# Kernel tuning notes

Measured on AMD Instinct MI355X. Metric: run time of the kernel, lower is better.

Reference implementation:

```python
import jax, jax.numpy as jnp
import numpy as np

N, M, D = 20000, 16000, 128

def setup_inputs() -> dict:
    key = jax.random.key(0)
    ks = jax.random.split(key, 4)
    return {
        "clear_feature": jax.random.normal(ks[0], (N, D), dtype=jnp.float32),
        "rain_feature": jax.random.normal(ks[1], (M, D), dtype=jnp.float32),
        # torch nn.Linear weight layout: (out_features, in_features)
        "W1": jax.random.normal(ks[2], (D, 2 * D), dtype=jnp.float32) * 0.05,
        "b1": jnp.zeros((D,), dtype=jnp.float32),
        "W2": jax.random.normal(ks[3], (1, D), dtype=jnp.float32) * 0.05,
        "b2": jnp.zeros((1,), dtype=jnp.float32),
    }

def reference(clear_feature, rain_feature, W1, b1, W2, b2):
    # --- KNN alignment (k=1): argmin of squared Euclidean distance == cdist+topk(smallest) ---
    x2 = jnp.sum(clear_feature * clear_feature, axis=-1, keepdims=True)   # [N,1]
    y2 = jnp.sum(rain_feature * rain_feature, axis=-1)                    # [M]
    d2 = x2 + y2 - 2.0 * (clear_feature @ rain_feature.T)                 # [N,M]
    idx = jnp.argmin(d2, axis=-1)                                         # [N]
    aligned = rain_feature[idx]                                           # [N,D] gather
    # --- attention MLP: Linear(2D->D) + ReLU + Linear(D->1) + Sigmoid ---
    comb = jnp.concatenate([clear_feature, aligned], axis=-1)             # [N,2D]
    h = jax.nn.relu(comb @ W1.T + b1)                                     # [N,D]
    w = jax.nn.sigmoid(h @ W2.T + b2)                                     # [N,1]
    # --- gated fusion ---
    return w * clear_feature + (1.0 - w) * aligned
```

## Files before the change

### kernel.cpp

```cpp
#include <hip/hip_runtime.h>
#include <stdint.h>

#define NN 20000
#define MM 16000
#define DD 128
#define CT 500
#define SPLITS 32
#define RBG 157

typedef unsigned long long u64;
typedef _Float16 f16x8 __attribute__((ext_vector_type(8)));
typedef float f32x16 __attribute__((ext_vector_type(16)));

__global__ void k_y2(const float* __restrict__ rain, float* __restrict__ y2) {
    int row = blockIdx.x * 4 + (threadIdx.x >> 6);
    int lane = threadIdx.x & 63;
    if (row >= MM) return;
    float2 v = ((const float2*)(rain + (size_t)row * DD))[lane];
    float s = v.x * v.x + v.y * v.y;
    #pragma unroll
    for (int off = 32; off > 0; off >>= 1) s += __shfl_down(s, off);
    if (lane == 0) y2[row] = s;
}

__global__ void k_split_B(const float* __restrict__ rain, _Float16* __restrict__ Bimg) {
    int id = blockIdx.x * 256 + threadIdx.x;
    if (id >= CT * 512) return;
    int cl = id & 31;
    int kh = (id >> 5) & 1;
    int ks = (id >> 6) & 7;
    int tc = id >> 9;
    int m = tc * 32 + cl;
    const float4* src = (const float4*)(rain + (size_t)m * DD + ks * 16 + kh * 8);
    float4 v0 = src[0], v1 = src[1];
    float x[8] = {v0.x, v0.y, v0.z, v0.w, v1.x, v1.y, v1.z, v1.w};
    _Float16 hi[8], lo[8];
    #pragma unroll
    for (int j = 0; j < 8; ++j) {
        _Float16 h = (_Float16)x[j];
        hi[j] = h;
        lo[j] = (_Float16)(x[j] - (float)h);
    }
    int chunk = (ks * 2 + kh) * 32 + cl;
    size_t base = (size_t)tc * 8192;
    *(f16x8*)(Bimg + base + (size_t)chunk * 8) = *(f16x8*)hi;
    *(f16x8*)(Bimg + base + 4096 + (size_t)chunk * 8) = *(f16x8*)lo;
}

__global__ void k_w1img(const float* __restrict__ W1, _Float16* __restrict__ W1img) {
    int id = blockIdx.x * 256 + threadIdx.x;
    if (id >= 4096) return;
    int cl = id & 31;
    int kh = (id >> 5) & 1;
    int cg = (id >> 6) & 3;
    int ks = id >> 8;
    int d = cg * 32 + cl;
    int k = ks * 16 + kh * 8;
    const float4* src = (const float4*)(W1 + (size_t)d * 256 + k);
    float4 v0 = src[0], v1 = src[1];
    float x[8] = {v0.x, v0.y, v0.z, v0.w, v1.x, v1.y, v1.z, v1.w};
    _Float16 h[8];
    #pragma unroll
    for (int j = 0; j < 8; ++j) h[j] = (_Float16)x[j];
    *(f16x8*)(W1img + (size_t)id * 8) = *(f16x8*)h;
}

__global__ __launch_bounds__(256, 3) void k_dist(
        const float* __restrict__ clear_f,
        const _Float16* __restrict__ Bimg, const float* __restrict__ y2,
        u64* __restrict__ keys2) {
    __shared__ _Float16 lds[2][8192];
    __shared__ float y2s[512];

    const int tid = threadIdx.x;
    const int w = tid >> 6, lane = tid & 63;
    const int l5 = lane >> 5, l31 = lane & 31;
    const int b = blockIdx.x;
    const int split = b & 31;
    const int n0 = (b >> 5) * 128;
    const int nt = (CT - split + SPLITS - 1) / SPLITS;

    #define STAGE(T, BUF) do {                                                 \
        const _Float16* gsrc_ = Bimg + (size_t)(T) * 8192;                     \
        _Float16* dst_ = &lds[BUF][0];                                         \
        _Pragma("unroll")                                                      \
        for (int n_ = 0; n_ < 4; ++n_) {                                       \
            int seg_ = w * 4 + n_;                                             \
            __builtin_amdgcn_global_load_lds(                                  \
                (const __attribute__((address_space(1))) unsigned int*)        \
                    (gsrc_ + (size_t)seg_ * 512 + (size_t)lane * 8),           \
                (__attribute__((address_space(3))) unsigned int*)              \
                    (dst_ + (size_t)seg_ * 512),                               \
                16, 0, 0);                                                     \
        }                                                                      \
    } while (0)

    STAGE(split, 0);

    for (int j = tid; j < nt * 32; j += 256) {
        int tt = j >> 5;
        int cc = j & 31;
        y2s[j] = y2[(split + tt * SPLITS) * 32 + cc];
    }

    f16x8 afh[8], afl[8];
    {
        int r = n0 + w * 32 + l31;
        if (r >= NN) r = NN - 1;
        const float* ap = clear_f + (size_t)r * DD + l5 * 8;
        #pragma unroll
        for (int ks = 0; ks < 8; ++ks) {
            float4 v0 = *(const float4*)(ap + ks * 16);
            float4 v1 = *(const float4*)(ap + ks * 16 + 4);
            float x[8] = {v0.x, v0.y, v0.z, v0.w, v1.x, v1.y, v1.z, v1.w};
            _Float16 hi[8], lo[8];
            #pragma unroll
            for (int j = 0; j < 8; ++j) {
                float s = -2.f * x[j];
                _Float16 h = (_Float16)s;
                hi[j] = h;
                lo[j] = (_Float16)(s - (float)h);
            }
            afh[ks] = *(f16x8*)hi;
            afl[ks] = *(f16x8*)lo;
        }
    }

    __syncthreads();

    float bestd[16];
    unsigned bits[2] = {0u, 0u};
    #pragma unroll
    for (int s = 0; s < 16; ++s) bestd[s] = 1e30f;

    int p = 0;
    for (int i = 0; i < nt; ++i) {
        if (i + 1 < nt) STAGE(split + (i + 1) * SPLITS, 1 - p);

        float y2v = y2s[i * 32 + l31];

        f32x16 accA, accB;
        #pragma unroll
        for (int e = 0; e < 16; ++e) { accA[e] = y2v; accB[e] = 0.f; }

        const _Float16* lbuf = &lds[p][0];
        #pragma unroll
        for (int ks = 0; ks < 8; ++ks) {
            f16x8 bh = *(const f16x8*)(lbuf + (size_t)ks * 512 + (size_t)lane * 8);
            f16x8 bl = *(const f16x8*)(lbuf + 4096 + (size_t)ks * 512 + (size_t)lane * 8);
            __builtin_amdgcn_s_setprio(1);
            accA = __builtin_amdgcn_mfma_f32_32x32x16_f16(afh[ks], bh, accA, 0, 0, 0);
            accB = __builtin_amdgcn_mfma_f32_32x32x16_f16(afl[ks], bh, accB, 0, 0, 0);
            accA = __builtin_amdgcn_mfma_f32_32x32x16_f16(afh[ks], bl, accA, 0, 0, 0);
            __builtin_amdgcn_s_setprio(0);
        }

        const unsigned nib = (unsigned)i;
        #pragma unroll
        for (int e = 0; e < 16; ++e) {
            float d = accA[e] + accB[e];
            int sh = 4 * (e & 7);
            bool up = d < bestd[e];
            bestd[e] = up ? d : bestd[e];
            bits[e >> 3] = up ? ((bits[e >> 3] & ~(15u << sh)) | (nib << sh))
                              : bits[e >> 3];
        }

        __syncthreads();
        p ^= 1;
    }
    #undef STAGE

    #pragma unroll
    for (int s = 0; s < 16; ++s) {
        unsigned nib = (bits[s >> 3] >> (4 * (s & 7))) & 15u;
        int col = (split + (int)nib * SPLITS) * 32 + l31;
        unsigned u = __float_as_uint(bestd[s]);
        u = (u & 0x80000000u) ? ~u : (u | 0x80000000u);
        u64 key = ((u64)u << 32) | (unsigned)col;
        #pragma unroll
        for (int off = 1; off < 32; off <<= 1) {
            u64 o = __shfl_xor(key, off);
            if (o < key) key = o;
        }
        if (l31 == 0) {
            int grow = n0 + w * 32 + (s & 3) + 8 * (s >> 2) + 4 * l5;
            if (grow < NN) keys2[(size_t)grow * SPLITS + split] = key;
        }
    }
}

__global__ void k_reduce(const u64* __restrict__ keys2, int* __restrict__ idx) {
    int gid = blockIdx.x * 256 + threadIdx.x;
    int row = gid >> 5, j = gid & 31;
    if (row >= NN) return;
    u64 k = keys2[(size_t)row * SPLITS + j];
    #pragma unroll
    for (int off = 16; off > 0; off >>= 1) {
        u64 o = __shfl_xor(k, off);
        if (o < k) k = o;
    }
    if (j == 0) idx[row] = (int)(k & 0xffffffffu);
}

__global__ __launch_bounds__(64) void k_mlp(
        const float* __restrict__ clear_f, const float* __restrict__ rain_f,
        const _Float16* __restrict__ W1img, const float* __restrict__ b1,
        const float* __restrict__ W2, const float* __restrict__ b2,
        const int* __restrict__ idx, float* __restrict__ out) {
    const int lane = threadIdx.x;
    const int l5 = lane >> 5, l31 = lane & 31;
    const int n0 = blockIdx.x * 32;

    int n = n0 + l31;
    int nc = n < NN ? n : NN - 1;
    int rid = idx[nc];
    f16x8 af[16];
    #pragma unroll
    for (int ks = 0; ks < 16; ++ks) {
        int k0 = ks * 16 + l5 * 8;
        const float4* src = (k0 < 128)
            ? (const float4*)(clear_f + (size_t)nc * DD + k0)
            : (const float4*)(rain_f + (size_t)rid * DD + (k0 - 128));
        float4 v0 = src[0], v1 = src[1];
        float x[8] = {v0.x, v0.y, v0.z, v0.w, v1.x, v1.y, v1.z, v1.w};
        _Float16 h[8];
        #pragma unroll
        for (int j = 0; j < 8; ++j) h[j] = (_Float16)x[j];
        af[ks] = *(f16x8*)h;
    }

    f32x16 acc[4];
    #pragma unroll
    for (int cg = 0; cg < 4; ++cg)
        #pragma unroll
        for (int e = 0; e < 16; ++e) acc[cg][e] = 0.f;

    #pragma unroll
    for (int ks = 0; ks < 16; ++ks) {
        #pragma unroll
        for (int cg = 0; cg < 4; ++cg) {
            f16x8 bh = *(const f16x8*)(W1img +
                ((size_t)((ks * 4 + cg) * 2 + l5)) * 256 + (size_t)l31 * 8);
            acc[cg] = __builtin_amdgcn_mfma_f32_32x32x16_f16(af[ks], bh, acc[cg], 0, 0, 0);
        }
    }

    float b1v[4], w2v[4];
    #pragma unroll
    for (int cg = 0; cg < 4; ++cg) {
        b1v[cg] = b1[cg * 32 + l31];
        w2v[cg] = W2[cg * 32 + l31];
    }
    float b2v = b2[0];

    #pragma unroll
    for (int e = 0; e < 16; ++e) {
        float part = 0.f;
        #pragma unroll
        for (int cg = 0; cg < 4; ++cg) {
            float hv = acc[cg][e] + b1v[cg];
            hv = hv > 0.f ? hv : 0.f;
            part = fmaf(hv, w2v[cg], part);
        }
        #pragma unroll
        for (int off = 1; off < 32; off <<= 1) part += __shfl_xor(part, off);
        float s = part + b2v;
        float wv = 1.f / (1.f + expf(-s));
        int row = n0 + (e & 3) + 8 * (e >> 2) + 4 * l5;
        if (row < NN) {
            int rid2 = idx[row];
            float4 cv = *(const float4*)(clear_f + (size_t)row * DD + l31 * 4);
            float4 av = *(const float4*)(rain_f + (size_t)rid2 * DD + l31 * 4);
            float4 ov;
            ov.x = wv * cv.x + (1.f - wv) * av.x;
            ov.y = wv * cv.y + (1.f - wv) * av.y;
            ov.z = wv * cv.z + (1.f - wv) * av.z;
            ov.w = wv * cv.w + (1.f - wv) * av.w;
            *(float4*)(out + (size_t)row * DD + l31 * 4) = ov;
        }
    }
}

extern "C" void kernel_launch(void* const* d_in, const int* in_sizes, int n_in,
                              void* d_out, int out_size, void* d_ws, size_t ws_size,
                              hipStream_t stream) {
    const float* clear_f = (const float*)d_in[0];
    const float* rain_f = (const float*)d_in[1];
    const float* W1 = (const float*)d_in[2];
    const float* b1 = (const float*)d_in[3];
    const float* W2 = (const float*)d_in[4];
    const float* b2 = (const float*)d_in[5];
    float* out = (float*)d_out;

    char* ws = (char*)d_ws;
    u64* keys2 = (u64*)ws;
    int* idx = (int*)(ws + 5120000);
    float* y2 = (float*)(ws + 5200000);
    _Float16* Bimg = (_Float16*)(ws + 5264000);
    _Float16* W1img = (_Float16*)(ws + 13456000);

    k_y2<<<MM / 4, 256, 0, stream>>>(rain_f, y2);
    k_split_B<<<(CT * 512 + 255) / 256, 256, 0, stream>>>(rain_f, Bimg);
    k_w1img<<<16, 256, 0, stream>>>(W1, W1img);
    k_dist<<<RBG * SPLITS, 256, 0, stream>>>(clear_f, Bimg, y2, keys2);
    k_reduce<<<(NN * 32 + 255) / 256, 256, 0, stream>>>(keys2, idx);
    k_mlp<<<(NN + 31) / 32, 64, 0, stream>>>(clear_f, rain_f, W1img, b1, W2, b2, idx, out);
}
```

Before: 357.3 us.

## Widen distance tile to 64 columns, halve splits, software-pipeline argmin fold

Each k_dist iteration now processes 64 rain columns, as two 32-wide MFMA accumulator pairs that reuse the same A fragments. The number of column splits drops from 32 to 16. The argmin fold of the previous tile is deferred so it overlaps the next tile's MFMAs, and the extra accB accumulator is removed by folding the lo term into the same accumulator. The goal is more MFMA work per LDS stage and barrier, plus less keys2 traffic and a cheaper reduce. In exchange it uses double the LDS and more registers, with occupancy lowered from 3 to 2 blocks per CU.

```diff
diff --git a/kernel.cpp b/kernel.cpp
--- a/kernel.cpp
+++ b/kernel.cpp
@@ -4,8 +4,8 @@
 #define NN 20000
 #define MM 16000
 #define DD 128
-#define CT 500
-#define SPLITS 32
+#define CT2 250
+#define SPLITS 16
 #define RBG 157
 
 typedef unsigned long long u64;
@@ -25,13 +25,13 @@
 
 __global__ void k_split_B(const float* __restrict__ rain, _Float16* __restrict__ Bimg) {
     int id = blockIdx.x * 256 + threadIdx.x;
-    if (id >= CT * 512) return;
+    if (id >= CT2 * 1024) return;
     int cl = id & 31;
-    int kh = (id >> 5) & 1;
-    int ks = (id >> 6) & 7;
-    int tc = id >> 9;
-    int m = tc * 32 + cl;
-    const float4* src = (const float4*)(rain + (size_t)m * DD + ks * 16 + kh * 8);
+    int cg = (id >> 5) & 1;
+    int kp = (id >> 6) & 15;
+    int tc = id >> 10;
+    int row = tc * 64 + cg * 32 + cl;
+    const float4* src = (const float4*)(rain + (size_t)row * DD + kp * 8);
     float4 v0 = src[0], v1 = src[1];
     float x[8] = {v0.x, v0.y, v0.z, v0.w, v1.x, v1.y, v1.z, v1.w};
     _Float16 hi[8], lo[8];
@@ -41,10 +41,11 @@
         hi[j] = h;
         lo[j] = (_Float16)(x[j] - (float)h);
     }
-    int chunk = (ks * 2 + kh) * 32 + cl;
-    size_t base = (size_t)tc * 8192;
+    int ks = kp >> 1, kh = kp & 1;
+    int chunk = ((ks * 2 + cg) * 2 + kh) * 32 + cl;
+    size_t base = (size_t)tc * 16384;
     *(f16x8*)(Bimg + base + (size_t)chunk * 8) = *(f16x8*)hi;
-    *(f16x8*)(Bimg + base + 4096 + (size_t)chunk * 8) = *(f16x8*)lo;
+    *(f16x8*)(Bimg + base + 8192 + (size_t)chunk * 8) = *(f16x8*)lo;
 }
 
 __global__ void k_w1img(const float* __restrict__ W1, _Float16* __restrict__ W1img) {
@@ -65,27 +66,27 @@
     *(f16x8*)(W1img + (size_t)id * 8) = *(f16x8*)h;
 }
 
-__global__ __launch_bounds__(256, 3) void k_dist(
+__global__ __launch_bounds__(256, 2) void k_dist(
         const float* __restrict__ clear_f,
         const _Float16* __restrict__ Bimg, const float* __restrict__ y2,
         u64* __restrict__ keys2) {
-    __shared__ _Float16 lds[2][8192];
-    __shared__ float y2s[512];
+    __shared__ _Float16 lds[2][16384];
+    __shared__ float y2s[1024];
 
     const int tid = threadIdx.x;
     const int w = tid >> 6, lane = tid & 63;
     const int l5 = lane >> 5, l31 = lane & 31;
     const int b = blockIdx.x;
-    const int split = b & 31;
-    const int n0 = (b >> 5) * 128;
-    const int nt = (CT - split + SPLITS - 1) / SPLITS;
+    const int split = b & 15;
+    const int n0 = (b >> 4) * 128;
+    const int nt = (CT2 - split + SPLITS - 1) / SPLITS;
 
     #define STAGE(T, BUF) do {                                                 \
-        const _Float16* gsrc_ = Bimg + (size_t)(T) * 8192;                     \
+        const _Float16* gsrc_ = Bimg + (size_t)(T) * 16384;                    \
         _Float16* dst_ = &lds[BUF][0];                                         \
         _Pragma("unroll")                                                      \
-        for (int n_ = 0; n_ < 4; ++n_) {                                       \
-            int seg_ = w * 4 + n_;                                             \
+        for (int n_ = 0; n_ < 8; ++n_) {                                       \
+            int seg_ = w * 8 + n_;                                             \
             __builtin_amdgcn_global_load_lds(                                  \
                 (const __attribute__((address_space(1))) unsigned int*)        \
                     (gsrc_ + (size_t)seg_ * 512 + (size_t)lane * 8),           \
@@ -97,10 +98,10 @@
 
     STAGE(split, 0);
 
-    for (int j = tid; j < nt * 32; j += 256) {
-        int tt = j >> 5;
-        int cc = j & 31;
-        y2s[j] = y2[(split + tt * SPLITS) * 32 + cc];
+    for (int j = tid; j < nt * 64; j += 256) {
+        int tt = j >> 6;
+        int cc = j & 63;
+        y2s[j] = y2[(split + tt * SPLITS) * 64 + cc];
     }
 
     f16x8 afh[8], afl[8];
@@ -129,52 +130,77 @@
     __syncthreads();
 
     float bestd[16];
-    unsigned bits[2] = {0u, 0u};
+    unsigned bits[4] = {0u, 0u, 0u, 0u};
     #pragma unroll
     for (int s = 0; s < 16; ++s) bestd[s] = 1e30f;
+
+    f32x16 eA0, eA1, oA0, oA1;
+
+    #define COMPUTE(I, A0, A1) do {                                            \
+        float y2v0_ = y2s[(I) * 64 + l31];                                     \
+        float y2v1_ = y2s[(I) * 64 + 32 + l31];                                \
+        _Pragma("unroll")                                                      \
+        for (int e_ = 0; e_ < 16; ++e_) { A0[e_] = y2v0_; A1[e_] = y2v1_; }    \
+        const _Float16* lbuf_ = &lds[p][0];                                    \
+        _Pragma("unroll")                                                      \
+        for (int ks_ = 0; ks_ < 8; ++ks_) {                                    \
+            f16x8 bh0_ = *(const f16x8*)(lbuf_ + (size_t)(ks_ * 2 + 0) * 512 + (size_t)lane * 8); \
+            f16x8 bh1_ = *(const f16x8*)(lbuf_ + (size_t)(ks_ * 2 + 1) * 512 + (size_t)lane * 8); \
+            f16x8 bl0_ = *(const f16x8*)(lbuf_ + 8192 + (size_t)(ks_ * 2 + 0) * 512 + (size_t)lane * 8); \
+            f16x8 bl1_ = *(const f16x8*)(lbuf_ + 8192 + (size_t)(ks_ * 2 + 1) * 512 + (size_t)lane * 8); \
+            __builtin_amdgcn_s_setprio(1);                                     \
+            A0 = __builtin_amdgcn_mfma_f32_32x32x16_f16(afh[ks_], bh0_, A0, 0, 0, 0); \
+            A1 = __builtin_amdgcn_mfma_f32_32x32x16_f16(afh[ks_], bh1_, A1, 0, 0, 0); \
+            A0 = __builtin_amdgcn_mfma_f32_32x32x16_f16(afl[ks_], bh0_, A0, 0, 0, 0); \
+            A1 = __builtin_amdgcn_mfma_f32_32x32x16_f16(afl[ks_], bh1_, A1, 0, 0, 0); \
+            A0 = __builtin_amdgcn_mfma_f32_32x32x16_f16(afh[ks_], bl0_, A0, 0, 0, 0); \
+            A1 = __builtin_amdgcn_mfma_f32_32x32x16_f16(afh[ks_], bl1_, A1, 0, 0, 0); \
+            __builtin_amdgcn_s_setprio(0);                                     \
+        }                                                                      \
+    } while (0)
+
+    #define FOLD(A0, A1, IDX) do {                                             \
+        const unsigned ibase_ = ((unsigned)(IDX)) << 1;                        \
+        _Pragma("unroll")                                                      \
+        for (int e_ = 0; e_ < 16; ++e_) {                                      \
+            float d0_ = A0[e_], d1_ = A1[e_];                                  \
+            bool tk_ = d1_ < d0_;                                              \
+            float dm_ = tk_ ? d1_ : d0_;                                       \
+            int sh_ = 8 * (e_ & 3);                                            \
+            bool up_ = dm_ < bestd[e_];                                        \
+            bestd[e_] = up_ ? dm_ : bestd[e_];                                 \
+            unsigned nib_ = ibase_ | (unsigned)tk_;                            \
+            bits[e_ >> 2] = up_ ? ((bits[e_ >> 2] & ~(255u << sh_)) | (nib_ << sh_)) \
+                                : bits[e_ >> 2];                               \
+        }                                                                      \
+    } while (0)
 
     int p = 0;
     for (int i = 0; i < nt; ++i) {
         if (i + 1 < nt) STAGE(split + (i + 1) * SPLITS, 1 - p);
 
-        float y2v = y2s[i * 32 + l31];
-
-        f32x16 accA, accB;
-        #pragma unroll
-        for (int e = 0; e < 16; ++e) { accA[e] = y2v; accB[e] = 0.f; }
-
-        const _Float16* lbuf = &lds[p][0];
-        #pragma unroll
-        for (int ks = 0; ks < 8; ++ks) {
-            f16x8 bh = *(const f16x8*)(lbuf + (size_t)ks * 512 + (size_t)lane * 8);
-            f16x8 bl = *(const f16x8*)(lbuf + 4096 + (size_t)ks * 512 + (size_t)lane * 8);
-            __builtin_amdgcn_s_setprio(1);
-            accA = __builtin_amdgcn_mfma_f32_32x32x16_f16(afh[ks], bh, accA, 0, 0, 0);
-            accB = __builtin_amdgcn_mfma_f32_32x32x16_f16(afl[ks], bh, accB, 0, 0, 0);
-            accA = __builtin_amdgcn_mfma_f32_32x32x16_f16(afh[ks], bl, accA, 0, 0, 0);
-            __builtin_amdgcn_s_setprio(0);
-        }
-
-        const unsigned nib = (unsigned)i;
-        #pragma unroll
-        for (int e = 0; e < 16; ++e) {
-            float d = accA[e] + accB[e];
-            int sh = 4 * (e & 7);
-            bool up = d < bestd[e];
-            bestd[e] = up ? d : bestd[e];
-            bits[e >> 3] = up ? ((bits[e >> 3] & ~(15u << sh)) | (nib << sh))
-                              : bits[e >> 3];
+        if ((i & 1) == 0) {
+            COMPUTE(i, eA0, eA1);
+            if (i > 0) FOLD(oA0, oA1, i - 1);
+        } else {
+            COMPUTE(i, oA0, oA1);
+            FOLD(eA0, eA1, i - 1);
         }
 
         __syncthreads();
         p ^= 1;
     }
+    if (nt & 1) FOLD(eA0, eA1, nt - 1);
+    else        FOLD(oA0, oA1, nt - 1);
+    #undef COMPUTE
+    #undef FOLD
     #undef STAGE
 
     #pragma unroll
     for (int s = 0; s < 16; ++s) {
-        unsigned nib = (bits[s >> 3] >> (4 * (s & 7))) & 15u;
-        int col = (split + (int)nib * SPLITS) * 32 + l31;
+        unsigned nib = (bits[s >> 2] >> (8 * (s & 3))) & 255u;
+        int i4 = (int)(nib >> 1), cg = (int)(nib & 1);
+        int col = (split + i4 * SPLITS) * 64 + cg * 32 + l31;
         unsigned u = __float_as_uint(bestd[s]);
         u = (u & 0x80000000u) ? ~u : (u | 0x80000000u);
         u64 key = ((u64)u << 32) | (unsigned)col;
@@ -192,12 +218,12 @@
 
 __global__ void k_reduce(const u64* __restrict__ keys2, int* __restrict__ idx) {
     int gid = blockIdx.x * 256 + threadIdx.x;
-    int row = gid >> 5, j = gid & 31;
+    int row = gid >> 4, j = gid & 15;
     if (row >= NN) return;
     u64 k = keys2[(size_t)row * SPLITS + j];
     #pragma unroll
-    for (int off = 16; off > 0; off >>= 1) {
-        u64 o = __shfl_xor(k, off);
+    for (int off = 8; off > 0; off >>= 1) {
+        u64 o = __shfl_xor(k, off, 16);
         if (o < k) k = o;
     }
     if (j == 0) idx[row] = (int)(k & 0xffffffffu);
@@ -295,15 +321,15 @@
 
     char* ws = (char*)d_ws;
     u64* keys2 = (u64*)ws;
-    int* idx = (int*)(ws + 5120000);
-    float* y2 = (float*)(ws + 5200000);
-    _Float16* Bimg = (_Float16*)(ws + 5264000);
-    _Float16* W1img = (_Float16*)(ws + 13456000);
+    int* idx = (int*)(ws + 2560000);
+    float* y2 = (float*)(ws + 2640000);
+    _Float16* Bimg = (_Float16*)(ws + 2704000);
+    _Float16* W1img = (_Float16*)(ws + 10896000);
 
     k_y2<<<MM / 4, 256, 0, stream>>>(rain_f, y2);
-    k_split_B<<<(CT * 512 + 255) / 256, 256, 0, stream>>>(rain_f, Bimg);
+    k_split_B<<<(CT2 * 1024 + 255) / 256, 256, 0, stream>>>(rain_f, Bimg);
     k_w1img<<<16, 256, 0, stream>>>(W1, W1img);
     k_dist<<<RBG * SPLITS, 256, 0, stream>>>(clear_f, Bimg, y2, keys2);
-    k_reduce<<<(NN * 32 + 255) / 256, 256, 0, stream>>>(keys2, idx);
+    k_reduce<<<(NN * SPLITS + 255) / 256, 256, 0, stream>>>(keys2, idx);
     k_mlp<<<(NN + 31) / 32, 64, 0, stream>>>(clear_f, rain_f, W1img, b1, W2, b2, idx, out);
 }
```

New measurement: 652.5 us. +82.6%, slower.
